# Kernel tuning notes

Measured on AMD Instinct MI355X. Metric: run time of the kernel, lower is better.

Reference implementation:

```python
import jax, jax.numpy as jnp
import numpy as np

N_NODES = 100000
N_EDGES = 3200000
IN_DIM = 62
OUT_DIM = 16
EDGE_DIM = 2


def setup_inputs() -> dict:
    key = jax.random.key(0)
    ks = jax.random.split(key, 8)
    h = jax.random.normal(ks[0], (N_NODES, IN_DIM), dtype=jnp.float32)
    e = jax.random.normal(ks[1], (N_EDGES, EDGE_DIM), dtype=jnp.float32)
    src = jax.random.randint(ks[2], (N_EDGES,), 0, N_NODES, dtype=jnp.int32)
    dst = jax.random.randint(ks[3], (N_EDGES,), 0, N_NODES, dtype=jnp.int32)
    # xavier-normal-ish scaled weights
    W_fc = jax.random.normal(ks[4], (OUT_DIM, IN_DIM), dtype=jnp.float32) * 0.2
    W_attn = jax.random.normal(ks[5], (1, 2 * OUT_DIM + EDGE_DIM), dtype=jnp.float32) * 0.2
    W_edge = jax.random.normal(ks[6], (EDGE_DIM, EDGE_DIM), dtype=jnp.float32) * 0.5
    W_e2n = jax.random.normal(ks[7], (OUT_DIM, EDGE_DIM), dtype=jnp.float32) * 0.5
    return {"h": h, "e": e, "src": src, "dst": dst, "W_fc": W_fc,
            "W_attn": W_attn, "W_edge": W_edge, "W_e2n": W_e2n}


def _agat_forward(h, e, src, dst, W_fc, W_attn, W_edge, W_e2n):
    n = h.shape[0]
    d = W_fc.shape[0]
    z = h @ W_fc.T                      # [N, D]
    ex = e @ W_edge.T                   # [E, edge_dim]
    # attn_fc([z_src, z_dst, ex]) split into per-part projections
    Wa_src = W_attn[:, :d]              # [1, D]
    Wa_dst = W_attn[:, d:2 * d]         # [1, D]
    Wa_e = W_attn[:, 2 * d:]            # [1, edge_dim]
    a_src = (z @ Wa_src.T)[:, 0]        # [N] per-node, gathered per-edge
    a_dst = (z @ Wa_dst.T)[:, 0]        # [N]
    a = a_src[src] + a_dst[dst] + (ex @ Wa_e.T)[:, 0]   # [E]
    e_att = jax.nn.leaky_relu(a, negative_slope=0.01)    # [E]
    # segment softmax over incoming edges of each dst node
    m = jax.ops.segment_max(e_att, dst, num_segments=n)  # [N]
    w = jnp.exp(e_att - m[dst])                           # [E]
    denom = jax.ops.segment_sum(w, dst, num_segments=n)   # [N]
    attn = w / denom[dst]                                  # [E]
    # message = z_src + ez; aggregated as attn-weighted sum (matches
    # sum(attn*z) + sum(attn*ez) in reduce_func)
    ez = ex @ W_e2n.T                                      # [E, D]
    msg = attn[:, None] * (z[src] + ez)                    # [E, D]
    return jax.ops.segment_sum(msg, dst, num_segments=n)   # [N, D]


def reference(h, e, src, dst, W_fc, W_attn, W_edge, W_e2n):
    return _agat_forward(h, e, src, dst, W_fc, W_attn, W_edge, W_e2n)
```

## Files before the change

kernel.cpp:

```cpp
#include <hip/hip_runtime.h>
#include <hip/hip_fp16.h>

#define N_NODES 100000
#define N_EDGES 3200000
#define IN_DIM  62
#define OUT_DIM 16

#define EBC    6144
#define EPT    (EBC / 1024)
#define NEB    ((N_EDGES + EBC - 1) / EBC)
#define NPB    ((N_NODES + 1023) / 1024)
#define NBUCK  ((N_NODES + 63) / 64)
#define CAPL   4096
#define CSTR   16

typedef int nat_i2 __attribute__((ext_vector_type(2)));

__global__ __launch_bounds__(1024) void proj_append_kernel(
    const float* __restrict__ h,
    const float* __restrict__ W_fc,
    const float* __restrict__ W_attn,
    const float* __restrict__ e,
    const int*   __restrict__ src,
    const int*   __restrict__ dst,
    __half* __restrict__ zh,
    float* __restrict__ a_src_arr,
    float* __restrict__ a_dst_arr,
    int*   __restrict__ cursor,
    nat_i2* __restrict__ records,
    int cap)
{
    __shared__ int  cnt[NBUCK];
    __shared__ int  pfx[NBUCK];
    __shared__ int  combo[NBUCK];
    __shared__ int2 pay[EBC];
    __shared__ unsigned short pbkt[EBC];
    __shared__ int  wsum[16];

    int tid = threadIdx.x;

    if (blockIdx.x < NPB) {
        int i = blockIdx.x * 1024 + tid;
        if (i >= N_NODES) return;

        float acc[OUT_DIM];
#pragma unroll
        for (int j = 0; j < OUT_DIM; ++j) acc[j] = 0.f;

        const float2* __restrict__ hr = (const float2*)(h + (size_t)i * IN_DIM);
#pragma unroll
        for (int kk = 0; kk < IN_DIM / 2; ++kk) {
            float2 hv = hr[kk];
#pragma unroll
            for (int j = 0; j < OUT_DIM; ++j) {
                acc[j] += hv.x * W_fc[j * IN_DIM + 2 * kk]
                        + hv.y * W_fc[j * IN_DIM + 2 * kk + 1];
            }
        }

        float asrc = 0.f, adst = 0.f;
#pragma unroll
        for (int j = 0; j < OUT_DIM; ++j) {
            asrc += acc[j] * W_attn[j];
            adst += acc[j] * W_attn[OUT_DIM + j];
        }

        union { __half hx[16]; uint4 q[2]; } u;
#pragma unroll
        for (int j = 0; j < OUT_DIM; ++j) u.hx[j] = __float2half(acc[j]);
        uint4* __restrict__ zrow = (uint4*)(zh + (size_t)i * OUT_DIM);
        zrow[0] = u.q[0];
        zrow[1] = u.q[1];

        a_src_arr[i] = asrc;
        a_dst_arr[i] = adst;
        return;
    }

    int be = blockIdx.x - NPB;
    long ebase = (long)be * EBC;
    int chunk_n = (int)min((long)EBC, (long)N_EDGES - ebase);

    int dv[EPT], sv[EPT];
    float2 ev[EPT];
#pragma unroll
    for (int j = 0; j < EPT; ++j) {
        int p = tid + j * 1024;
        dv[j] = -1;
        if (p < chunk_n) {
            long eid = ebase + p;
            dv[j] = dst[eid];
            sv[j] = src[eid];
            ev[j] = ((const float2*)e)[eid];
        }
    }

    for (int t = tid; t < NBUCK; t += 1024) cnt[t] = 0;
    __syncthreads();

#pragma unroll
    for (int j = 0; j < EPT; ++j)
        if (dv[j] >= 0) atomicAdd(&cnt[dv[j] >> 6], 1);
    __syncthreads();

    int b0 = 2 * tid, b1 = b0 + 1;
    int c0 = (b0 < NBUCK) ? cnt[b0] : 0;
    int c1 = (b1 < NBUCK) ? cnt[b1] : 0;
    if (b0 < NBUCK) cnt[b0] = 0;
    if (b1 < NBUCK) cnt[b1] = 0;
    int gb0 = 0, gb1 = 0;
    if (c0) gb0 = atomicAdd(&cursor[b0 * CSTR], c0);
    if (c1) gb1 = atomicAdd(&cursor[b1 * CSTR], c1);

    int ts = c0 + c1;
    {
        int lane = tid & 63, wid = tid >> 6;
        int x = ts;
#pragma unroll
        for (int off = 1; off < 64; off <<= 1) {
            int y = __shfl_up(x, off, 64);
            if (lane >= off) x += y;
        }
        if (lane == 63) wsum[wid] = x;
        __syncthreads();
        if (wid == 0) {
            int v = (lane < 16) ? wsum[lane] : 0;
#pragma unroll
            for (int off = 1; off < 16; off <<= 1) {
                int y = __shfl_up(v, off, 64);
                if (lane >= off) v += y;
            }
            if (lane < 16) wsum[lane] = v;
        }
        __syncthreads();
        int texcl = x - ts + (wid ? wsum[wid - 1] : 0);
        if (b0 < NBUCK) { pfx[b0] = texcl;      combo[b0] = b0 * cap + gb0 - texcl; }
        if (b1 < NBUCK) { pfx[b1] = texcl + c0; combo[b1] = b1 * cap + gb1 - (texcl + c0); }
    }
    __syncthreads();

#pragma unroll
    for (int j = 0; j < EPT; ++j) {
        if (dv[j] >= 0) {
            int b = dv[j] >> 6;
            union { __half2 h2; int i; } uu;
            uu.h2.x = __float2half(ev[j].x);
            uu.h2.y = __float2half(ev[j].y);
            int r = atomicAdd(&cnt[b], 1);
            int q = pfx[b] + r;
            pay[q]  = make_int2(uu.i, sv[j] | ((dv[j] & 63) << 17));
            pbkt[q] = (unsigned short)b;
        }
    }
    __syncthreads();

    for (int p = tid; p < chunk_n; p += 1024) {
        int2 v = pay[p];
        int bb = pbkt[p];
        int pos = combo[bb] + p;
        if (pos < (bb + 1) * cap) {
            nat_i2 vv; vv.x = v.x; vv.y = v.y;
            __builtin_nontemporal_store(vv, records + pos);
        }
    }
}

__global__ __launch_bounds__(1024) void bucket_gather_kernel(
    const int*    __restrict__ cursor,
    const nat_i2* __restrict__ records,
    const __half* __restrict__ zh,
    const float*  __restrict__ a_src_arr,
    const float*  __restrict__ a_dst_arr,
    const float*  __restrict__ W_attn,
    const float*  __restrict__ W_edge,
    const float*  __restrict__ W_e2n,
    float* __restrict__ out, int cap)
{
    __shared__ int2 rec[CAPL];
    __shared__ unsigned short inv[CAPL];
    __shared__ unsigned int exb[CAPL];
    __shared__ int hist[64], pfx[64], cur[64];
    __shared__ float adst_l[64];

    int b   = blockIdx.x;
    int tid = threadIdx.x;
    long lo = (long)b * cap;
    int n   = cursor[b * CSTR];
    int nl  = n < cap ? n : cap;
    if (nl > CAPL) nl = CAPL;

    if (tid < 64) {
        hist[tid] = 0; cur[tid] = 0;
        int node = (b << 6) + tid;
        adst_l[tid] = (node < N_NODES) ? a_dst_arr[node] : 0.f;
    }
    __syncthreads();

    float we00 = W_edge[0], we01 = W_edge[1], we10 = W_edge[2], we11 = W_edge[3];
    float wa0  = W_attn[2 * OUT_DIM], wa1 = W_attn[2 * OUT_DIM + 1];

    int ld0 = -1, ld1 = -1, ld2 = -1, ld3 = -1;
#define EDGEW(J, LD)                                                        \
    {                                                                       \
        int k = tid + (J) * 1024;                                           \
        if (k < nl) {                                                       \
            nat_i2 r = __builtin_nontemporal_load(records + lo + k);        \
            int s  = r.y & 0x1FFFF;                                         \
            LD     = (r.y >> 17) & 63;                                      \
            union { int i; __half2 h2; } ue; ue.i = r.x;                    \
            float e0 = __low2float(ue.h2), e1 = __high2float(ue.h2);        \
            float ex0 = e0 * we00 + e1 * we01;                              \
            float ex1 = e0 * we10 + e1 * we11;                              \
            float a = a_src_arr[s] + adst_l[LD] + ex0 * wa0 + ex1 * wa1;    \
            float ea = (a > 0.f) ? a : 0.01f * a;                           \
            float w  = __expf(ea);                                          \
            rec[k] = make_int2(__float_as_int(w), r.y);                     \
            union { unsigned int i; __half2 h2; } up;                       \
            up.h2.x = __float2half(ex0);                                    \
            up.h2.y = __float2half(ex1);                                    \
            exb[k] = up.i;                                                  \
            atomicAdd(&hist[LD], 1);                                        \
        }                                                                   \
    }
    EDGEW(0, ld0) EDGEW(1, ld1) EDGEW(2, ld2) EDGEW(3, ld3)
#undef EDGEW
    __syncthreads();

    if (tid < 64) pfx[tid] = hist[tid];
    __syncthreads();
    for (int off = 1; off < 64; off <<= 1) {
        int t = 0;
        if (tid < 64 && tid >= off) t = pfx[tid - off];
        __syncthreads();
        if (tid < 64) pfx[tid] += t;
        __syncthreads();
    }
    if (tid < 64) pfx[tid] -= hist[tid];
    __syncthreads();

#define INVW(J, LD)                                                         \
    if (LD >= 0) {                                                          \
        int k = tid + (J) * 1024;                                           \
        int r = atomicAdd(&cur[LD], 1);                                     \
        inv[pfx[LD] + r] = (unsigned short)k;                               \
    }
    INVW(0, ld0) INVW(1, ld1) INVW(2, ld2) INVW(3, ld3)
#undef INVW
    __syncthreads();

    int ld   = tid >> 4;
    int lane = tid & 15;
    int node = (b << 6) + ld;
    if (node >= N_NODES) return;

    int m    = hist[ld];
    int base = pfx[ld];

    float acc0 = 0.f, acc1 = 0.f, accw0 = 0.f, accw1 = 0.f;
    float ax00 = 0.f, ax01 = 0.f, ax10 = 0.f, ax11 = 0.f;

    int i = 0;
    for (; i + 1 < m; i += 2) {
        int k0 = inv[base + i];
        int k1 = inv[base + i + 1];
        int2 r0 = rec[k0];
        int2 r1 = rec[k1];
        float w0 = __int_as_float(r0.x);
        float w1 = __int_as_float(r1.x);
        int s0 = r0.y & 0x1FFFF;
        int s1 = r1.y & 0x1FFFF;
        union { unsigned int i; __half2 h2; } x0, x1;
        x0.i = exb[k0];
        x1.i = exb[k1];

        float zv0 = __half2float(zh[s0 * OUT_DIM + lane]);
        float zv1 = __half2float(zh[s1 * OUT_DIM + lane]);

        acc0  += w0 * zv0;                 acc1  += w1 * zv1;
        accw0 += w0;                       accw1 += w1;
        ax00  += w0 * __low2float(x0.h2);  ax01  += w1 * __low2float(x1.h2);
        ax10  += w0 * __high2float(x0.h2); ax11  += w1 * __high2float(x1.h2);
    }
    if (i < m) {
        int k0 = inv[base + i];
        int2 r0 = rec[k0];
        float w0 = __int_as_float(r0.x);
        int s0 = r0.y & 0x1FFFF;
        union { unsigned int i; __half2 h2; } x0;
        x0.i = exb[k0];
        float zv0 = __half2float(zh[s0 * OUT_DIM + lane]);
        acc0  += w0 * zv0;
        accw0 += w0;
        ax00  += w0 * __low2float(x0.h2);
        ax10  += w0 * __high2float(x0.h2);
    }

    float acc  = acc0 + acc1;
    float accw = accw0 + accw1;
    float ax0  = ax00 + ax01;
    float ax1  = ax10 + ax11;

    float ez   = ax0 * W_e2n[2 * lane] + ax1 * W_e2n[2 * lane + 1];
    float invw = (accw != 0.f) ? (1.f / accw) : 0.f;
    out[(size_t)node * OUT_DIM + lane] = (acc + ez) * invw;
}


__global__ __launch_bounds__(256) void node_proj_fb_kernel(
    const float* __restrict__ h,
    const float* __restrict__ W_fc,
    const float* __restrict__ W_attn,
    float* __restrict__ z,
    float* __restrict__ a_src_arr,
    float* __restrict__ a_dst_arr,
    float* __restrict__ denom,
    float* __restrict__ out)
{
    int i = blockIdx.x * blockDim.x + threadIdx.x;
    if (i >= N_NODES) return;

    float acc[OUT_DIM];
#pragma unroll
    for (int j = 0; j < OUT_DIM; ++j) acc[j] = 0.f;

    const float2* __restrict__ hr = (const float2*)(h + (size_t)i * IN_DIM);
#pragma unroll
    for (int kk = 0; kk < IN_DIM / 2; ++kk) {
        float2 hv = hr[kk];
#pragma unroll
        for (int j = 0; j < OUT_DIM; ++j) {
            acc[j] += hv.x * W_fc[j * IN_DIM + 2 * kk]
                    + hv.y * W_fc[j * IN_DIM + 2 * kk + 1];
        }
    }

    float asrc = 0.f, adst = 0.f;
#pragma unroll
    for (int j = 0; j < OUT_DIM; ++j) {
        asrc += acc[j] * W_attn[j];
        adst += acc[j] * W_attn[OUT_DIM + j];
    }

    float4* __restrict__ zrow = (float4*)(z + (size_t)i * OUT_DIM);
    zrow[0] = make_float4(acc[0],  acc[1],  acc[2],  acc[3]);
    zrow[1] = make_float4(acc[4],  acc[5],  acc[6],  acc[7]);
    zrow[2] = make_float4(acc[8],  acc[9],  acc[10], acc[11]);
    zrow[3] = make_float4(acc[12], acc[13], acc[14], acc[15]);

    a_src_arr[i] = asrc;
    a_dst_arr[i] = adst;
    denom[i] = 0.f;

    float4 z4 = make_float4(0.f, 0.f, 0.f, 0.f);
    float4* __restrict__ orow = (float4*)(out + (size_t)i * OUT_DIM);
    orow[0] = z4; orow[1] = z4; orow[2] = z4; orow[3] = z4;
}

__global__ __launch_bounds__(256) void edge_kernel(
    const float* __restrict__ e,
    const int*   __restrict__ src,
    const int*   __restrict__ dst,
    const float* __restrict__ W_attn,
    const float* __restrict__ W_edge,
    const float* __restrict__ W_e2n,
    const float* __restrict__ z,
    const float* __restrict__ a_src_arr,
    const float* __restrict__ a_dst_arr,
    float* __restrict__ denom,
    float* __restrict__ out)
{
    int eid = blockIdx.x * blockDim.x + threadIdx.x;
    if (eid >= N_EDGES) return;

    int s = src[eid];
    int d = dst[eid];

    float2 ev = ((const float2*)e)[eid];
    float ex0 = ev.x * W_edge[0] + ev.y * W_edge[1];
    float ex1 = ev.x * W_edge[2] + ev.y * W_edge[3];

    float a = a_src_arr[s] + a_dst_arr[d]
            + ex0 * W_attn[2 * OUT_DIM] + ex1 * W_attn[2 * OUT_DIM + 1];
    float ea = (a > 0.f) ? a : 0.01f * a;
    float w  = __expf(ea);

    unsafeAtomicAdd(denom + d, w);

    const float4* __restrict__ zrow = (const float4*)(z + (size_t)s * OUT_DIM);
    float4 z0 = zrow[0], z1 = zrow[1], z2 = zrow[2], z3 = zrow[3];

    float* __restrict__ orow = out + (size_t)d * OUT_DIM;
    float zs[OUT_DIM] = { z0.x, z0.y, z0.z, z0.w,
                          z1.x, z1.y, z1.z, z1.w,
                          z2.x, z2.y, z2.z, z2.w,
                          z3.x, z3.y, z3.z, z3.w };
#pragma unroll
    for (int j = 0; j < OUT_DIM; ++j) {
        float ez = ex0 * W_e2n[2 * j] + ex1 * W_e2n[2 * j + 1];
        unsafeAtomicAdd(orow + j, w * (zs[j] + ez));
    }
}

__global__ __launch_bounds__(256) void normalize_kernel(
    float* __restrict__ out, const float* __restrict__ denom)
{
    int tid = blockIdx.x * blockDim.x + threadIdx.x;
    const int total = N_NODES * OUT_DIM / 4;
    if (tid >= total) return;
    int n = tid >> 2;
    float dn = denom[n];
    float inv = (dn != 0.f) ? (1.f / dn) : 0.f;
    float4 v = ((float4*)out)[tid];
    v.x *= inv; v.y *= inv; v.z *= inv; v.w *= inv;
    ((float4*)out)[tid] = v;
}

extern "C" void kernel_launch(void* const* d_in, const int* in_sizes, int n_in,
                              void* d_out, int out_size, void* d_ws, size_t ws_size,
                              hipStream_t stream)
{
    const float* h      = (const float*)d_in[0];
    const float* e      = (const float*)d_in[1];
    const int*   src    = (const int*)  d_in[2];
    const int*   dst    = (const int*)  d_in[3];
    const float* W_fc   = (const float*)d_in[4];
    const float* W_attn = (const float*)d_in[5];
    const float* W_edge = (const float*)d_in[6];
    const float* W_e2n  = (const float*)d_in[7];
    float* out = (float*)d_out;

    char* ws = (char*)d_ws;

    size_t off = 0;
    __half* zh        = (__half*)(ws + off); off += (size_t)N_NODES * OUT_DIM * 2;
    float*  a_src_arr = (float*) (ws + off); off += (size_t)N_NODES * 4;
    float*  a_dst_arr = (float*) (ws + off); off += (size_t)N_NODES * 4;
    int*    cursor    = (int*)   (ws + off); off += (size_t)NBUCK * CSTR * 4;
    size_t rec_off = (off + 255) & ~(size_t)255;

    int cap = 0;
    if      (ws_size >= rec_off + (size_t)NBUCK * 4096 * 8) cap = 4096;
    else if (ws_size >= rec_off + (size_t)NBUCK * 3072 * 8) cap = 3072;
    else if (ws_size >= rec_off + (size_t)NBUCK * 2560 * 8) cap = 2560;
    else if (ws_size >= rec_off + (size_t)NBUCK * 2304 * 8) cap = 2304;

    if (cap) {
        nat_i2* records = (nat_i2*)(ws + rec_off);

        hipMemsetAsync(cursor, 0, (size_t)NBUCK * CSTR * sizeof(int), stream);

        proj_append_kernel<<<NPB + NEB, 1024, 0, stream>>>(
            h, W_fc, W_attn, e, src, dst,
            zh, a_src_arr, a_dst_arr, cursor, records, cap);

        bucket_gather_kernel<<<NBUCK, 1024, 0, stream>>>(
            cursor, records, zh, a_src_arr, a_dst_arr,
            W_attn, W_edge, W_e2n, out, cap);
    } else {
        size_t foff = 0;
        float* z     = (float*)(ws + foff); foff += (size_t)N_NODES * OUT_DIM * 4;
        float* asrc  = (float*)(ws + foff); foff += (size_t)N_NODES * 4;
        float* adst  = (float*)(ws + foff); foff += (size_t)N_NODES * 4;
        float* denom = (float*)(ws + foff); foff += (size_t)N_NODES * 4;

        node_proj_fb_kernel<<<(N_NODES + 255) / 256, 256, 0, stream>>>(
            h, W_fc, W_attn, z, asrc, adst, denom, out);

        edge_kernel<<<(N_EDGES + 255) / 256, 256, 0, stream>>>(
            e, src, dst, W_attn, W_edge, W_e2n, z, asrc, adst, denom, out);

        normalize_kernel<<<(N_NODES * OUT_DIM / 4 + 255) / 256, 256, 0, stream>>>(
            out, denom);
    }
}
```

Measured before the change: 220.5 us.

## Replace per-bucket LDS sort with fixed-point atomic accumulation in gather

The gather kernel no longer counting-sorts edges by destination in shared memory. It makes two passes over the bucket's records. The first pass computes per-node maxima with integer atomicMax on order-preserving float keys. The second pass accumulates the exp-weighted z rows, the weight sum and the edge features into shared-memory integer accumulators using fixed-point scaling and atomicAdd. This removes the histogram, prefix scan, inverse index and the large LDS buffers, at the cost of 19 LDS atomics per edge, recomputing the attention logit, and a risk of fixed-point overflow or precision loss. It also adds max subtraction for numerical stability.

```diff
diff --git a/kernel.cpp b/kernel.cpp
--- a/kernel.cpp
+++ b/kernel.cpp
@@ -11,10 +11,21 @@
 #define NEB    ((N_EDGES + EBC - 1) / EBC)
 #define NPB    ((N_NODES + 1023) / 1024)
 #define NBUCK  ((N_NODES + 63) / 64)
-#define CAPL   4096
 #define CSTR   16
+#define ACCS   21
+#define SZF    1048576.0f
+#define SWF    16777216.0f
 
 typedef int nat_i2 __attribute__((ext_vector_type(2)));
+
+__device__ __forceinline__ unsigned fkey(float f) {
+    unsigned b = __float_as_uint(f);
+    return (b & 0x80000000u) ? ~b : (b | 0x80000000u);
+}
+__device__ __forceinline__ float finv(unsigned u) {
+    unsigned b = (u & 0x80000000u) ? (u ^ 0x80000000u) : ~u;
+    return __uint_as_float(b);
+}
 
 __global__ __launch_bounds__(1024) void proj_append_kernel(
     const float* __restrict__ h,
@@ -165,7 +176,7 @@
     }
 }
 
-__global__ __launch_bounds__(1024) void bucket_gather_kernel(
+__global__ __launch_bounds__(1024) void gather_fx_kernel(
     const int*    __restrict__ cursor,
     const nat_i2* __restrict__ records,
     const __half* __restrict__ zh,
@@ -176,133 +187,97 @@
     const float*  __restrict__ W_e2n,
     float* __restrict__ out, int cap)
 {
-    __shared__ int2 rec[CAPL];
-    __shared__ unsigned short inv[CAPL];
-    __shared__ unsigned int exb[CAPL];
-    __shared__ int hist[64], pfx[64], cur[64];
-    __shared__ float adst_l[64];
+    __shared__ unsigned maxv[64];
+    __shared__ int      acci[64 * ACCS];
+    __shared__ float    adst_l[64];
+    __shared__ float    we2n_s[2 * OUT_DIM];
 
     int b   = blockIdx.x;
     int tid = threadIdx.x;
     long lo = (long)b * cap;
     int n   = cursor[b * CSTR];
     int nl  = n < cap ? n : cap;
-    if (nl > CAPL) nl = CAPL;
 
     if (tid < 64) {
-        hist[tid] = 0; cur[tid] = 0;
+        maxv[tid] = 0u;
         int node = (b << 6) + tid;
         adst_l[tid] = (node < N_NODES) ? a_dst_arr[node] : 0.f;
     }
+    if (tid < 2 * OUT_DIM) we2n_s[tid] = W_e2n[tid];
+    for (int t = tid; t < 64 * ACCS; t += 1024) acci[t] = 0;
     __syncthreads();
 
     float we00 = W_edge[0], we01 = W_edge[1], we10 = W_edge[2], we11 = W_edge[3];
     float wa0  = W_attn[2 * OUT_DIM], wa1 = W_attn[2 * OUT_DIM + 1];
 
-    int ld0 = -1, ld1 = -1, ld2 = -1, ld3 = -1;
-#define EDGEW(J, LD)                                                        \
-    {                                                                       \
-        int k = tid + (J) * 1024;                                           \
-        if (k < nl) {                                                       \
-            nat_i2 r = __builtin_nontemporal_load(records + lo + k);        \
-            int s  = r.y & 0x1FFFF;                                         \
-            LD     = (r.y >> 17) & 63;                                      \
-            union { int i; __half2 h2; } ue; ue.i = r.x;                    \
-            float e0 = __low2float(ue.h2), e1 = __high2float(ue.h2);        \
-            float ex0 = e0 * we00 + e1 * we01;                              \
-            float ex1 = e0 * we10 + e1 * we11;                              \
-            float a = a_src_arr[s] + adst_l[LD] + ex0 * wa0 + ex1 * wa1;    \
-            float ea = (a > 0.f) ? a : 0.01f * a;                           \
-            float w  = __expf(ea);                                          \
-            rec[k] = make_int2(__float_as_int(w), r.y);                     \
-            union { unsigned int i; __half2 h2; } up;                       \
-            up.h2.x = __float2half(ex0);                                    \
-            up.h2.y = __float2half(ex1);                                    \
-            exb[k] = up.i;                                                  \
-            atomicAdd(&hist[LD], 1);                                        \
-        }                                                                   \
-    }
-    EDGEW(0, ld0) EDGEW(1, ld1) EDGEW(2, ld2) EDGEW(3, ld3)
-#undef EDGEW
-    __syncthreads();
-
-    if (tid < 64) pfx[tid] = hist[tid];
-    __syncthreads();
-    for (int off = 1; off < 64; off <<= 1) {
-        int t = 0;
-        if (tid < 64 && tid >= off) t = pfx[tid - off];
-        __syncthreads();
-        if (tid < 64) pfx[tid] += t;
-        __syncthreads();
-    }
-    if (tid < 64) pfx[tid] -= hist[tid];
-    __syncthreads();
-
-#define INVW(J, LD)                                                         \
-    if (LD >= 0) {                                                          \
-        int k = tid + (J) * 1024;                                           \
-        int r = atomicAdd(&cur[LD], 1);                                     \
-        inv[pfx[LD] + r] = (unsigned short)k;                               \
-    }
-    INVW(0, ld0) INVW(1, ld1) INVW(2, ld2) INVW(3, ld3)
-#undef INVW
-    __syncthreads();
-
-    int ld   = tid >> 4;
-    int lane = tid & 15;
-    int node = (b << 6) + ld;
-    if (node >= N_NODES) return;
-
-    int m    = hist[ld];
-    int base = pfx[ld];
-
-    float acc0 = 0.f, acc1 = 0.f, accw0 = 0.f, accw1 = 0.f;
-    float ax00 = 0.f, ax01 = 0.f, ax10 = 0.f, ax11 = 0.f;
-
-    int i = 0;
-    for (; i + 1 < m; i += 2) {
-        int k0 = inv[base + i];
-        int k1 = inv[base + i + 1];
-        int2 r0 = rec[k0];
-        int2 r1 = rec[k1];
-        float w0 = __int_as_float(r0.x);
-        float w1 = __int_as_float(r1.x);
-        int s0 = r0.y & 0x1FFFF;
-        int s1 = r1.y & 0x1FFFF;
-        union { unsigned int i; __half2 h2; } x0, x1;
-        x0.i = exb[k0];
-        x1.i = exb[k1];
-
-        float zv0 = __half2float(zh[s0 * OUT_DIM + lane]);
-        float zv1 = __half2float(zh[s1 * OUT_DIM + lane]);
-
-        acc0  += w0 * zv0;                 acc1  += w1 * zv1;
-        accw0 += w0;                       accw1 += w1;
-        ax00  += w0 * __low2float(x0.h2);  ax01  += w1 * __low2float(x1.h2);
-        ax10  += w0 * __high2float(x0.h2); ax11  += w1 * __high2float(x1.h2);
-    }
-    if (i < m) {
-        int k0 = inv[base + i];
-        int2 r0 = rec[k0];
-        float w0 = __int_as_float(r0.x);
-        int s0 = r0.y & 0x1FFFF;
-        union { unsigned int i; __half2 h2; } x0;
-        x0.i = exb[k0];
-        float zv0 = __half2float(zh[s0 * OUT_DIM + lane]);
-        acc0  += w0 * zv0;
-        accw0 += w0;
-        ax00  += w0 * __low2float(x0.h2);
-        ax10  += w0 * __high2float(x0.h2);
-    }
-
-    float acc  = acc0 + acc1;
-    float accw = accw0 + accw1;
-    float ax0  = ax00 + ax01;
-    float ax1  = ax10 + ax11;
-
-    float ez   = ax0 * W_e2n[2 * lane] + ax1 * W_e2n[2 * lane + 1];
-    float invw = (accw != 0.f) ? (1.f / accw) : 0.f;
-    out[(size_t)node * OUT_DIM + lane] = (acc + ez) * invw;
+    for (int k = tid; k < nl; k += 1024) {
+        nat_i2 r = records[lo + k];
+        int s  = r.y & 0x1FFFF;
+        int ld = (r.y >> 17) & 63;
+        union { int i; __half2 h2; } ue; ue.i = r.x;
+        float e0 = __low2float(ue.h2), e1 = __high2float(ue.h2);
+        float ex0 = e0 * we00 + e1 * we01;
+        float ex1 = e0 * we10 + e1 * we11;
+        float a  = a_src_arr[s] + adst_l[ld] + ex0 * wa0 + ex1 * wa1;
+        float ea = (a > 0.f) ? a : 0.01f * a;
+        atomicMax(&maxv[ld], fkey(ea));
+    }
+    __syncthreads();
+
+    for (int k = tid; k < nl; k += 1024) {
+        nat_i2 r = records[lo + k];
+        int s  = r.y & 0x1FFFF;
+        int ld = (r.y >> 17) & 63;
+        union { int i; __half2 h2; } ue; ue.i = r.x;
+        float e0 = __low2float(ue.h2), e1 = __high2float(ue.h2);
+        float ex0 = e0 * we00 + e1 * we01;
+        float ex1 = e0 * we10 + e1 * we11;
+        float a  = a_src_arr[s] + adst_l[ld] + ex0 * wa0 + ex1 * wa1;
+        float ea = (a > 0.f) ? a : 0.01f * a;
+        float m  = finv(maxv[ld]);
+        float w  = __expf(ea - m);
+
+        const uint4* __restrict__ zr = (const uint4*)(zh + (size_t)s * OUT_DIM);
+        uint4 z0 = zr[0], z1 = zr[1];
+
+        int* ab = acci + ld * ACCS;
+        union { unsigned u; __half2 h2; } t2;
+        float ws = w * SZF;
+        t2.u = z0.x; atomicAdd(ab + 0,  __float2int_rn(ws * __low2float(t2.h2)));
+                     atomicAdd(ab + 1,  __float2int_rn(ws * __high2float(t2.h2)));
+        t2.u = z0.y; atomicAdd(ab + 2,  __float2int_rn(ws * __low2float(t2.h2)));
+                     atomicAdd(ab + 3,  __float2int_rn(ws * __high2float(t2.h2)));
+        t2.u = z0.z; atomicAdd(ab + 4,  __float2int_rn(ws * __low2float(t2.h2)));
+                     atomicAdd(ab + 5,  __float2int_rn(ws * __high2float(t2.h2)));
+        t2.u = z0.w; atomicAdd(ab + 6,  __float2int_rn(ws * __low2float(t2.h2)));
+                     atomicAdd(ab + 7,  __float2int_rn(ws * __high2float(t2.h2)));
+        t2.u = z1.x; atomicAdd(ab + 8,  __float2int_rn(ws * __low2float(t2.h2)));
+                     atomicAdd(ab + 9,  __float2int_rn(ws * __high2float(t2.h2)));
+        t2.u = z1.y; atomicAdd(ab + 10, __float2int_rn(ws * __low2float(t2.h2)));
+                     atomicAdd(ab + 11, __float2int_rn(ws * __high2float(t2.h2)));
+        t2.u = z1.z; atomicAdd(ab + 12, __float2int_rn(ws * __low2float(t2.h2)));
+                     atomicAdd(ab + 13, __float2int_rn(ws * __high2float(t2.h2)));
+        t2.u = z1.w; atomicAdd(ab + 14, __float2int_rn(ws * __low2float(t2.h2)));
+                     atomicAdd(ab + 15, __float2int_rn(ws * __high2float(t2.h2)));
+        atomicAdd(ab + 16, __float2int_rn(w * SWF));
+        atomicAdd(ab + 17, __float2int_rn(ws * ex0));
+        atomicAdd(ab + 18, __float2int_rn(ws * ex1));
+    }
+    __syncthreads();
+
+    int ln   = tid >> 4;
+    int j    = tid & 15;
+    int node = (b << 6) + ln;
+    if (node < N_NODES) {
+        const int* ab = acci + ln * ACCS;
+        int swi = ab[16];
+        float num  = (float)ab[j]  * (1.f / SZF);
+        float ex0s = (float)ab[17] * (1.f / SZF);
+        float ex1s = (float)ab[18] * (1.f / SZF);
+        float ez   = ex0s * we2n_s[2 * j] + ex1s * we2n_s[2 * j + 1];
+        float iv   = (swi != 0) ? (SWF / (float)swi) : 0.f;
+        out[(size_t)node * OUT_DIM + j] = (num + ez) * iv;
+    }
 }
 
 
@@ -435,7 +410,10 @@
     __half* zh        = (__half*)(ws + off); off += (size_t)N_NODES * OUT_DIM * 2;
     float*  a_src_arr = (float*) (ws + off); off += (size_t)N_NODES * 4;
     float*  a_dst_arr = (float*) (ws + off); off += (size_t)N_NODES * 4;
-    int*    cursor    = (int*)   (ws + off); off += (size_t)NBUCK * CSTR * 4;
+    off = (off + 255) & ~(size_t)255;
+    int*    cursor = (int*)(ws + off);
+    size_t  cur_bytes = (size_t)NBUCK * CSTR * 4;
+    off += (cur_bytes + 255) & ~(size_t)255;
     size_t rec_off = (off + 255) & ~(size_t)255;
 
     int cap = 0;
@@ -447,13 +425,13 @@
     if (cap) {
         nat_i2* records = (nat_i2*)(ws + rec_off);
 
-        hipMemsetAsync(cursor, 0, (size_t)NBUCK * CSTR * sizeof(int), stream);
+        hipMemsetAsync(cursor, 0, cur_bytes, stream);
 
         proj_append_kernel<<<NPB + NEB, 1024, 0, stream>>>(
             h, W_fc, W_attn, e, src, dst,
             zh, a_src_arr, a_dst_arr, cursor, records, cap);
 
-        bucket_gather_kernel<<<NBUCK, 1024, 0, stream>>>(
+        gather_fx_kernel<<<NBUCK, 1024, 0, stream>>>(
             cursor, records, zh, a_src_arr, a_dst_arr,
             W_attn, W_edge, W_e2n, out, cap);
     } else {
```

Measured after the change: 219.6 us. About the same (-0.4%).
